# Kernel tuning notes

Hardware: AMD Instinct MI355X
Metric: run time of the kernel (lower is better)

The kernel has to match this reference:

```python
import jax, jax.numpy as jnp
import numpy as np

KS = 3
PAD = 1
N = KS * KS  # 9 sampling points per output location


def setup_inputs() -> dict:
    key = jax.random.key(0)
    k1, k2, k3 = jax.random.split(key, 3)
    b, c, H, W, outc = 4, 128, 64, 64, 128
    x = jax.random.normal(k1, (b, c, H, W), jnp.float32)
    offset = jax.random.normal(k2, (b, 2 * N, H, W), jnp.float32)
    weight = jax.random.normal(k3, (outc, c, KS, KS), jnp.float32) * 0.05
    return {"x": x, "offset": offset, "weight": weight}


def reference(x, offset, weight):
    b, c, H, W = x.shape
    h, w = offset.shape[2], offset.shape[3]
    # reorder interleaved (x,y,x,y,...) offset channels to (all x, all y)
    idx = jnp.concatenate([jnp.arange(0, 2 * N, 2), jnp.arange(1, 2 * N, 2)])
    offset = offset[:, idx]
    # zero padding
    xp = jnp.pad(x, ((0, 0), (0, 0), (PAD, PAD), (PAD, PAD)))
    Hp, Wp = H + 2 * PAD, W + 2 * PAD
    # kernel-relative offsets p_n: [1, 2N, 1, 1]
    r = np.arange(-(KS - 1) // 2, (KS - 1) // 2 + 1)
    pnx, pny = np.meshgrid(r, r, indexing='ij')
    p_n = jnp.asarray(np.concatenate([pnx.flatten(), pny.flatten()]).reshape(1, 2 * N, 1, 1), jnp.float32)
    # base grid p_0: [1, 2N, h, w], coords start at 1 (padded frame)
    p0x, p0y = np.meshgrid(np.arange(1, h + 1), np.arange(1, w + 1), indexing='ij')
    p_0 = jnp.asarray(np.concatenate([np.tile(p0x.reshape(1, 1, h, w), (1, N, 1, 1)),
                                      np.tile(p0y.reshape(1, 1, h, w), (1, N, 1, 1))], axis=1), jnp.float32)
    p = jnp.transpose(p_0 + p_n + offset, (0, 2, 3, 1))  # [b, h, w, 2N]
    px, py = p[..., :N], p[..., N:]
    fx, fy = jnp.floor(px), jnp.floor(py)
    # 4 corner integer coords, clamped to padded image
    q_lt_x = jnp.clip(fx, 0, Hp - 1).astype(jnp.int32)
    q_lt_y = jnp.clip(fy, 0, Wp - 1).astype(jnp.int32)
    q_rb_x = jnp.clip(fx + 1, 0, Hp - 1).astype(jnp.int32)
    q_rb_y = jnp.clip(fy + 1, 0, Wp - 1).astype(jnp.int32)
    # out-of-range mask: snap p to floor(p) there (matches original, incl. zero grad thru floor)
    mask_x = jax.lax.stop_gradient(((px < PAD) | (px > Hp - 1 - PAD)).astype(px.dtype))
    mask_y = jax.lax.stop_gradient(((py < PAD) | (py > Wp - 1 - PAD)).astype(py.dtype))
    px = px * (1 - mask_x) + fx * mask_x
    py = py * (1 - mask_y) + fy * mask_y
    px = jnp.clip(px, 0, Hp - 1)
    py = jnp.clip(py, 0, Wp - 1)
    qltx = q_lt_x.astype(px.dtype); qlty = q_lt_y.astype(px.dtype)
    qrbx = q_rb_x.astype(px.dtype); qrby = q_rb_y.astype(px.dtype)
    # bilinear weights: [b, h, w, N]
    g_lt = (1 + (qltx - px)) * (1 + (qlty - py))
    g_rb = (1 - (qrbx - px)) * (1 - (qrby - py))
    g_lb = (1 + (qltx - px)) * (1 - (qrby - py))
    g_rt = (1 - (qrbx - px)) * (1 + (qlty - py))

    xv = xp.reshape(b, c, Hp * Wp)

    def gather(qx, qy):
        lin = (qx * Wp + qy).reshape(b, 1, h * w * N)
        g = jnp.take_along_axis(xv, jnp.broadcast_to(lin, (b, c, h * w * N)), axis=2)
        return g.reshape(b, c, h, w, N)

    x_off = (g_lt[:, None] * gather(q_lt_x, q_lt_y)
             + g_rb[:, None] * gather(q_rb_x, q_rb_y)
             + g_lb[:, None] * gather(q_lt_x, q_rb_y)
             + g_rt[:, None] * gather(q_rb_x, q_lt_y))  # [b, c, h, w, N]
    # N = i*ks + j -> out[(h,i),(w,j)]
    xo = x_off.reshape(b, c, h, w, KS, KS).transpose(0, 1, 2, 4, 3, 5).reshape(b, c, h * KS, w * KS)
    out = jax.lax.conv_general_dilated(xo, weight, window_strides=(KS, KS), padding='VALID',
                                       dimension_numbers=('NCHW', 'OIHW', 'NCHW'))
    return out
```

## Files before the change

### kernel.cpp

```cpp
#include <hip/hip_runtime.h>


typedef __bf16  v8bf16 __attribute__((ext_vector_type(8)));
typedef __bf16  bf16x2 __attribute__((ext_vector_type(2)));
typedef __bf16  bf16x4 __attribute__((ext_vector_type(4)));
typedef float   f32x4  __attribute__((ext_vector_type(4)));
typedef unsigned short ushort4v __attribute__((ext_vector_type(4)));
typedef _Float16 half4v __attribute__((ext_vector_type(4)));

#define CIN  128
#define NPT  9
#define KTOT 1152
#define OC   128
#define PX   32
#define NDESC (NPT * PX)
#define KSTEPS 36
#define KSC  12
#define LDBc 392
#define DTOT (9 * 4 * 64 * 64)
#define PXR  64
#define LDR  392

#define PB_WFRAG 72
#define PB_XPOSE 1024
#define PB_DESC  576
#define PB_ZERO  2048
#define PB_TOTAL (PB_WFRAG + PB_XPOSE + PB_DESC + PB_ZERO)

__device__ __forceinline__ void desc_compute(const float* __restrict__ off, int t,
                                             uint4* __restrict__ desc) {
    int j   = t & 63;
    int i   = (t >> 6) & 63;
    int b   = (t >> 12) & 3;
    int tap = t >> 14;

    float ox = off[(((b * 18) + 2 * tap) << 12) + (i << 6) + j];
    float oy = off[(((b * 18) + 2 * tap + 1) << 12) + (i << 6) + j];
    float px = (float)(i + tap / 3) + ox;
    float py = (float)(j + tap % 3) + oy;
    float fx = floorf(px), fy = floorf(py);
    int qltx = (int)fminf(fmaxf(fx, 0.f), 65.f);
    int qlty = (int)fminf(fmaxf(fy, 0.f), 65.f);
    int qrbx = (int)fminf(fmaxf(fx + 1.f, 0.f), 65.f);
    int qrby = (int)fminf(fmaxf(fy + 1.f, 0.f), 65.f);
    if (px < 1.f || px > 64.f) px = fx;
    if (py < 1.f || py > 64.f) py = fy;
    px = fminf(fmaxf(px, 0.f), 65.f);
    py = fminf(fmaxf(py, 0.f), 65.f);
    float wxl = 1.f + (float)qltx - px;
    float wxr = 1.f - ((float)qrbx - px);
    float wyl = 1.f + (float)qlty - py;
    float wyr = 1.f - ((float)qrby - py);
    float g[4] = { wxl * wyl, wxr * wyr, wxl * wyr, wxr * wyl };
    int qx[4] = { qltx, qrbx, qltx, qrbx };
    int qy[4] = { qlty, qrby, qrby, qlty };
    unsigned short idx[4];
    half4v gh;
    #pragma unroll
    for (int cr = 0; cr < 4; ++cr) {
        bool inb = (qx[cr] >= 1) && (qx[cr] <= 64) && (qy[cr] >= 1) && (qy[cr] <= 64);
        idx[cr] = inb ? (unsigned short)((qx[cr] - 1) * 64 + (qy[cr] - 1)) : 0;
        gh[cr]  = inb ? (_Float16)g[cr] : (_Float16)0.f;
    }
    uint4 rec;
    rec.x = (unsigned)idx[0] | ((unsigned)idx[1] << 16);
    rec.y = (unsigned)idx[2] | ((unsigned)idx[3] << 16);
    __builtin_memcpy(&rec.z, &gh, 8);
    int d = (((b << 6) + i) * 64 + j) * 9 + tap;
    desc[d] = rec;
}

__global__ __launch_bounds__(256) void prep_kernel(
    const float* __restrict__ x, const float* __restrict__ off,
    const float* __restrict__ w, __bf16* __restrict__ wfrag,
    __bf16* __restrict__ xt, uint4* __restrict__ desc,
    float* __restrict__ out)
{
    __shared__ float tile[64][33];
    const int bid = blockIdx.x;
    const int tid = threadIdx.x;

    if (bid < PB_WFRAG) {
        int t = bid * 256 + tid;
        if (t < 8 * KSTEPS * 64) {
            int lane = t & 63;
            int ks   = (t >> 6) % KSTEPS;
            int ot   = t / (KSTEPS * 64);
            int o    = ot * 16 + (lane & 15);
            v8bf16 frag;
            #pragma unroll
            for (int e = 0; e < 8; ++e) {
                int k   = ks * 32 + (lane >> 4) * 8 + e;
                int tap = k >> 7, c = k & 127;
                frag[e] = (__bf16)w[(size_t)o * KTOT + c * NPT + tap];
            }
            *(v8bf16*)(wfrag + (size_t)t * 8) = frag;
        }
    } else if (bid < PB_WFRAG + PB_XPOSE) {
        const int bidx = bid - PB_WFRAG;
        const int b   = bidx >> 8;
        const int hw0 = ((bidx >> 2) & 63) * 64;
        const int c0  = (bidx & 3) * 32;
        #pragma unroll
        for (int r = 0; r < 8; ++r) {
            int c_l  = (tid >> 6) + r * 4;
            int hw_l = tid & 63;
            tile[hw_l][c_l] = x[((size_t)(b * CIN + c0 + c_l) << 12) + hw0 + hw_l];
        }
        __syncthreads();
        #pragma unroll
        for (int r = 0; r < 8; ++r) {
            int hw_l = (tid >> 5) + r * 8;
            int c_l  = tid & 31;
            xt[((size_t)(b * 4096 + hw0 + hw_l)) * CIN + c0 + c_l] = (__bf16)tile[hw_l][c_l];
        }
    } else if (bid < PB_WFRAG + PB_XPOSE + PB_DESC) {
        int t = (bid - PB_WFRAG - PB_XPOSE) * 256 + tid;
        if (t < DTOT) desc_compute(off, t, desc);
    } else {
        int t = (bid - PB_WFRAG - PB_XPOSE - PB_DESC) * 256 + tid;
        f32x4 z = {0.f, 0.f, 0.f, 0.f};
        *(f32x4*)(out + (size_t)t * 4) = z;
    }
}

__global__ __launch_bounds__(512, 6) void splitk_kernel(
    const uint4* __restrict__ desc, const __bf16* __restrict__ xt,
    const __bf16* __restrict__ wfrag, float* __restrict__ out)
{
    __shared__ __align__(16) __bf16 Bt[PXR][LDR];

    const int bidx = blockIdx.x;
    const int kh3 = bidx % 3;
    const int rest = bidx / 3;
    const int i   = rest & 63;
    const int b   = rest >> 6;
    const int tid = threadIdx.x;

    const int tap0 = kh3 * 3;

    const int l  = tid & 63;
    const int wv = tid >> 6;

    const __bf16* xtb = xt + (((size_t)b << 12) * CIN);
    const int pix_base = ((b << 6) + i) * 64;

    const int hh = l >> 5;
    const int ll = l & 31;
    #pragma unroll 3
    for (int m = 0; m < 12; ++m) {
        int dl = wv * 24 + 2 * m + hh;
        int tap_l = dl >> 6, p = dl & 63;
        int d = (pix_base + p) * 9 + tap0 + tap_l;
        uint4 q = desc[d];
        unsigned short idx[4] = { (unsigned short)(q.x & 0xffff), (unsigned short)(q.x >> 16),
                                  (unsigned short)(q.y & 0xffff), (unsigned short)(q.y >> 16) };
        half4v gh;
        __builtin_memcpy(&gh, &q.z, 8);
        float s0 = 0.f, s1 = 0.f, s2 = 0.f, s3 = 0.f;
        #pragma unroll
        for (int cr = 0; cr < 4; ++cr) {
            uint2 v = *(const uint2*)(xtb + (size_t)idx[cr] * CIN + 4 * ll);
            float c0v, c1v, c2v, c3v;
            unsigned int l0 = v.x << 16, h0 = v.x & 0xffff0000u;
            unsigned int l1 = v.y << 16, h1 = v.y & 0xffff0000u;
            __builtin_memcpy(&c0v, &l0, 4);
            __builtin_memcpy(&c1v, &h0, 4);
            __builtin_memcpy(&c2v, &l1, 4);
            __builtin_memcpy(&c3v, &h1, 4);
            float gf = (float)gh[cr];
            s0 += gf * c0v;
            s1 += gf * c1v;
            s2 += gf * c2v;
            s3 += gf * c3v;
        }
        bf16x4 pr = { (__bf16)s0, (__bf16)s1, (__bf16)s2, (__bf16)s3 };
        *(bf16x4*)&Bt[p][tap_l * CIN + 4 * ll] = pr;
    }
    __syncthreads();

    const int quad = l >> 4;
    const int lr   = l & 15;

    f32x4 acc0 = {0.f, 0.f, 0.f, 0.f};
    f32x4 acc1 = {0.f, 0.f, 0.f, 0.f};
    f32x4 acc2 = {0.f, 0.f, 0.f, 0.f};
    f32x4 acc3 = {0.f, 0.f, 0.f, 0.f};

    const __bf16* brow0 = &Bt[lr][quad * 8];
    const __bf16* brow1 = &Bt[16 + lr][quad * 8];
    const __bf16* brow2 = &Bt[32 + lr][quad * 8];
    const __bf16* brow3 = &Bt[48 + lr][quad * 8];

    #pragma unroll 3
    for (int ks = 0; ks < KSC; ++ks) {
        int ks_g = kh3 * KSC + ks;
        v8bf16 afrag = *(const v8bf16*)(wfrag + (((size_t)wv * KSTEPS + ks_g) * 64 + l) * 8);
        v8bf16 b0 = *(const v8bf16*)(brow0 + ks * 32);
        v8bf16 b1 = *(const v8bf16*)(brow1 + ks * 32);
        v8bf16 b2 = *(const v8bf16*)(brow2 + ks * 32);
        v8bf16 b3 = *(const v8bf16*)(brow3 + ks * 32);
        acc0 = __builtin_amdgcn_mfma_f32_16x16x32_bf16(afrag, b0, acc0, 0, 0, 0);
        acc1 = __builtin_amdgcn_mfma_f32_16x16x32_bf16(afrag, b1, acc1, 0, 0, 0);
        acc2 = __builtin_amdgcn_mfma_f32_16x16x32_bf16(afrag, b2, acc2, 0, 0, 0);
        acc3 = __builtin_amdgcn_mfma_f32_16x16x32_bf16(afrag, b3, acc3, 0, 0, 0);
    }

    int obase = wv * 16 + quad * 4;
    float* opb = out + (((size_t)(b * OC + obase)) << 12) + (i << 6) + lr;
    #pragma unroll
    for (int ph = 0; ph < 4; ++ph) {
        f32x4 a = (ph == 0) ? acc0 : (ph == 1) ? acc1 : (ph == 2) ? acc2 : acc3;
        float* op = opb + ph * 16;
        #pragma unroll
        for (int r = 0; r < 4; ++r)
            unsafeAtomicAdd(op + ((size_t)r << 12), a[r]);
    }
}

__global__ __launch_bounds__(512, 8) void deform_fused_kernel(
    const float* __restrict__ x, const float* __restrict__ off,
    const float* __restrict__ w, const __bf16* __restrict__ wfrag,
    const __bf16* __restrict__ xt, float* __restrict__ out, int mode)
{
    __shared__ __align__(16) __bf16 Bt[PX][LDBc];
    __shared__ __align__(8)  unsigned short sIdxP[NDESC][4];
    __shared__ __align__(8)  _Float16      sGP[NDESC][4];

    const int bidx = blockIdx.x;
    const int b   = bidx >> 8;
    const int i   = (bidx >> 2) & 63;
    const int j0  = ((bidx >> 1) & 1) * PX;
    const int oh  = bidx & 1;
    const int tid = threadIdx.x;

    if (tid < NDESC) {
        int k = tid >> 5, p = tid & 31;
        int j = j0 + p;
        float ox = off[(((b * 18) + 2 * k) * 64 + i) * 64 + j];
        float oy = off[(((b * 18) + 2 * k + 1) * 64 + i) * 64 + j];
        float px = (float)(i + k / 3) + ox;
        float py = (float)(j + k % 3) + oy;
        float fx = floorf(px), fy = floorf(py);
        int qltx = (int)fminf(fmaxf(fx, 0.f), 65.f);
        int qlty = (int)fminf(fmaxf(fy, 0.f), 65.f);
        int qrbx = (int)fminf(fmaxf(fx + 1.f, 0.f), 65.f);
        int qrby = (int)fminf(fmaxf(fy + 1.f, 0.f), 65.f);
        if (px < 1.f || px > 64.f) px = fx;
        if (py < 1.f || py > 64.f) py = fy;
        px = fminf(fmaxf(px, 0.f), 65.f);
        py = fminf(fmaxf(py, 0.f), 65.f);
        float wxl = 1.f + (float)qltx - px;
        float wxr = 1.f - ((float)qrbx - px);
        float wyl = 1.f + (float)qlty - py;
        float wyr = 1.f - ((float)qrby - py);
        float g[4] = { wxl * wyl, wxr * wyr, wxl * wyr, wxr * wyl };
        int qx[4] = { qltx, qrbx, qltx, qrbx };
        int qy[4] = { qlty, qrby, qrby, qlty };
        #pragma unroll
        for (int cr = 0; cr < 4; ++cr) {
            bool inb = (qx[cr] >= 1) && (qx[cr] <= 64) && (qy[cr] >= 1) && (qy[cr] <= 64);
            sIdxP[tid][cr] = inb ? (unsigned short)((qx[cr] - 1) * 64 + (qy[cr] - 1)) : 0;
            sGP[tid][cr]   = inb ? (_Float16)g[cr] : (_Float16)0.f;
        }
    }
    __syncthreads();

    const int l    = tid & 63;
    const int wv   = tid >> 6;
    const int ot   = oh * 4 + (wv & 3);
    const int ph   = wv >> 2;
    const int quad = l >> 4;
    const int lr   = l & 15;

    f32x4 acc = {0.f, 0.f, 0.f, 0.f};
    const __bf16* xtb = xt + ((size_t)b * 4096) * CIN;
    const float*  xb  = x + ((size_t)b * CIN << 12);
    const __bf16* brow = &Bt[ph * 16 + lr][quad * 8];

    for (int t = 0; t < 3; ++t) {
        if (mode == 2) {
            #pragma unroll 4
            for (int dd = 0; dd < KSC; ++dd) {
                int dl = wv * KSC + dd;
                int tap_l = dl >> 5, p = dl & 31;
                int d = t * 96 + dl;
                ushort4v id = *(const ushort4v*)&sIdxP[d][0];
                half4v   gh = *(const half4v*)&sGP[d][0];
                float s0 = 0.f, s1 = 0.f;
                #pragma unroll
                for (int cr = 0; cr < 4; ++cr) {
                    unsigned int v = *(const unsigned int*)(xtb + (size_t)id[cr] * CIN + 2 * l);
                    float c0v, c1v;
                    unsigned int lo = v << 16, hi = v & 0xffff0000u;
                    __builtin_memcpy(&c0v, &lo, 4);
                    __builtin_memcpy(&c1v, &hi, 4);
                    float gf = (float)gh[cr];
                    s0 += gf * c0v;
                    s1 += gf * c1v;
                }
                bf16x2 pr = { (__bf16)s0, (__bf16)s1 };
                *(bf16x2*)&Bt[p][tap_l * CIN + 2 * l] = pr;
            }
        } else {
            for (int dd = 0; dd < KSC; ++dd) {
                int dl = wv * KSC + dd;
                int tap_l = dl >> 5, p = dl & 31;
                int d = t * 96 + dl;
                ushort4v id = *(const ushort4v*)&sIdxP[d][0];
                half4v   gh = *(const half4v*)&sGP[d][0];
                float s0 = 0.f, s1 = 0.f;
                #pragma unroll
                for (int cr = 0; cr < 4; ++cr) {
                    float gf = (float)gh[cr];
                    s0 += gf * xb[((size_t)(2 * l) << 12) + id[cr]];
                    s1 += gf * xb[((size_t)(2 * l + 1) << 12) + id[cr]];
                }
                bf16x2 pr = { (__bf16)s0, (__bf16)s1 };
                *(bf16x2*)&Bt[p][tap_l * CIN + 2 * l] = pr;
            }
        }
        __syncthreads();

        #pragma unroll 4
        for (int ks = 0; ks < KSC; ++ks) {
            int ks_g = t * KSC + ks;
            v8bf16 bfrag = *(const v8bf16*)(brow + ks * 32);
            v8bf16 afrag;
            if (mode >= 1) {
                afrag = *(const v8bf16*)(wfrag + (((size_t)ot * KSTEPS + ks_g) * 64 + l) * 8);
            } else {
                int o = ot * 16 + lr;
                #pragma unroll
                for (int e = 0; e < 8; ++e) {
                    int k = ks_g * 32 + quad * 8 + e;
                    int tap = k >> 7, c = k & 127;
                    afrag[e] = (__bf16)w[(size_t)o * KTOT + c * NPT + tap];
                }
            }
            acc = __builtin_amdgcn_mfma_f32_16x16x32_bf16(afrag, bfrag, acc, 0, 0, 0);
        }
        if (t < 2) __syncthreads();
    }

    {
        int obase = ot * 16 + quad * 4;
        float* op = out + (((size_t)(b * OC + obase)) << 12) + (i << 6) + j0 + ph * 16 + lr;
        #pragma unroll
        for (int r = 0; r < 4; ++r)
            op[(size_t)r << 12] = acc[r];
    }
}

__global__ __launch_bounds__(256) void wfrag_kernel(const float* __restrict__ w,
                                                    __bf16* __restrict__ wfrag) {
    int t = blockIdx.x * 256 + threadIdx.x;
    if (t >= 8 * KSTEPS * 64) return;
    int lane = t & 63;
    int ks   = (t >> 6) % KSTEPS;
    int ot   = t / (KSTEPS * 64);
    int o    = ot * 16 + (lane & 15);
    v8bf16 frag;
    #pragma unroll
    for (int e = 0; e < 8; ++e) {
        int k   = ks * 32 + (lane >> 4) * 8 + e;
        int tap = k >> 7, c = k & 127;
        frag[e] = (__bf16)w[(size_t)o * KTOT + c * NPT + tap];
    }
    *(v8bf16*)(wfrag + (size_t)t * 8) = frag;
}

__global__ __launch_bounds__(256) void xpose_kernel(const float* __restrict__ x,
                                                    __bf16* __restrict__ xt) {
    __shared__ float tile[64][33];
    const int bidx = blockIdx.x;
    const int b   = bidx >> 8;
    const int hw0 = ((bidx >> 2) & 63) * 64;
    const int c0  = (bidx & 3) * 32;
    const int tid = threadIdx.x;
    #pragma unroll
    for (int r = 0; r < 8; ++r) {
        int c_l  = (tid >> 6) + r * 4;
        int hw_l = tid & 63;
        tile[hw_l][c_l] = x[((size_t)(b * CIN + c0 + c_l) << 12) + hw0 + hw_l];
    }
    __syncthreads();
    #pragma unroll
    for (int r = 0; r < 8; ++r) {
        int hw_l = (tid >> 5) + r * 8;
        int c_l  = tid & 31;
        xt[((size_t)(b * 4096 + hw0 + hw_l)) * CIN + c0 + c_l] = (__bf16)tile[hw_l][c_l];
    }
}

extern "C" void kernel_launch(void* const* d_in, const int* in_sizes, int n_in,
                              void* d_out, int out_size, void* d_ws, size_t ws_size,
                              hipStream_t stream) {
    const float* x   = (const float*)d_in[0];
    const float* off = (const float*)d_in[1];
    const float* w   = (const float*)d_in[2];
    float* out = (float*)d_out;

    const size_t wfrag_bytes = (size_t)OC * KTOT * sizeof(__bf16);
    const size_t xt_bytes    = (size_t)4 * 4096 * CIN * sizeof(__bf16);
    const size_t desc_bytes  = (size_t)DTOT * 16;

    int mode = 0;
    if (ws_size >= wfrag_bytes + xt_bytes + desc_bytes) mode = 3;
    else if (ws_size >= wfrag_bytes + xt_bytes) mode = 2;
    else if (ws_size >= wfrag_bytes) mode = 1;

    __bf16* wfrag = (__bf16*)d_ws;
    __bf16* xt    = (__bf16*)((char*)d_ws + wfrag_bytes);
    uint4*  desc  = (uint4*) ((char*)d_ws + wfrag_bytes + xt_bytes);

    if (mode == 3) {
        prep_kernel<<<PB_TOTAL, 256, 0, stream>>>(x, off, w, wfrag, xt, desc, out);
        splitk_kernel<<<4 * 64 * 3, 512, 0, stream>>>(desc, xt, wfrag, out);
    } else {
        if (mode >= 1)
            wfrag_kernel<<<(8 * KSTEPS * 64 + 255) / 256, 256, 0, stream>>>(w, wfrag);
        if (mode >= 2)
            xpose_kernel<<<4 * 64 * 4, 256, 0, stream>>>(x, xt);
        deform_fused_kernel<<<4 * 64 * 2 * 2, 512, 0, stream>>>(x, off, w, wfrag, xt, out, mode);
    }
}
```

Baseline: 101.7 us.

## Widen gather loads to 16B, prefetch descriptors, and remap block order by batch

The gather phase now has each lane load 8 bf16 channels (16-byte loads) instead of 4, so 16 lanes cover one descriptor and the loop runs 6 iterations instead of 12. All 6 descriptors are loaded up front to raise memory-level parallelism. Block indices are remapped so adjacent blocks interleave batches differently, which is meant to change L2 locality across the grid. The costs are more registers (six uint4 descriptors plus eight accumulators per lane) and possible occupancy loss under launch_bounds(512,6).

```diff
diff --git a/kernel.cpp b/kernel.cpp
--- a/kernel.cpp
+++ b/kernel.cpp
@@ -3,7 +3,6 @@
 
 typedef __bf16  v8bf16 __attribute__((ext_vector_type(8)));
 typedef __bf16  bf16x2 __attribute__((ext_vector_type(2)));
-typedef __bf16  bf16x4 __attribute__((ext_vector_type(4)));
 typedef float   f32x4  __attribute__((ext_vector_type(4)));
 typedef unsigned short ushort4v __attribute__((ext_vector_type(4)));
 typedef _Float16 half4v __attribute__((ext_vector_type(4)));
@@ -131,11 +130,11 @@
     __shared__ __align__(16) __bf16 Bt[PXR][LDR];
 
     const int bidx = blockIdx.x;
-    const int kh3 = bidx % 3;
-    const int rest = bidx / 3;
-    const int i   = rest & 63;
-    const int b   = rest >> 6;
-    const int tid = threadIdx.x;
+    const int b    = (bidx & 7) >> 1;
+    const int sub  = ((bidx >> 3) << 1) | (bidx & 1);
+    const int kh3  = sub % 3;
+    const int i    = sub / 3;
+    const int tid  = threadIdx.x;
 
     const int tap0 = kh3 * 3;
 
@@ -145,37 +144,51 @@
     const __bf16* xtb = xt + (((size_t)b << 12) * CIN);
     const int pix_base = ((b << 6) + i) * 64;
 
-    const int hh = l >> 5;
-    const int ll = l & 31;
-    #pragma unroll 3
-    for (int m = 0; m < 12; ++m) {
-        int dl = wv * 24 + 2 * m + hh;
-        int tap_l = dl >> 6, p = dl & 63;
-        int d = (pix_base + p) * 9 + tap0 + tap_l;
-        uint4 q = desc[d];
-        unsigned short idx[4] = { (unsigned short)(q.x & 0xffff), (unsigned short)(q.x >> 16),
-                                  (unsigned short)(q.y & 0xffff), (unsigned short)(q.y >> 16) };
-        half4v gh;
-        __builtin_memcpy(&gh, &q.z, 8);
-        float s0 = 0.f, s1 = 0.f, s2 = 0.f, s3 = 0.f;
-        #pragma unroll
-        for (int cr = 0; cr < 4; ++cr) {
-            uint2 v = *(const uint2*)(xtb + (size_t)idx[cr] * CIN + 4 * ll);
-            float c0v, c1v, c2v, c3v;
-            unsigned int l0 = v.x << 16, h0 = v.x & 0xffff0000u;
-            unsigned int l1 = v.y << 16, h1 = v.y & 0xffff0000u;
-            __builtin_memcpy(&c0v, &l0, 4);
-            __builtin_memcpy(&c1v, &h0, 4);
-            __builtin_memcpy(&c2v, &l1, 4);
-            __builtin_memcpy(&c3v, &h1, 4);
-            float gf = (float)gh[cr];
-            s0 += gf * c0v;
-            s1 += gf * c1v;
-            s2 += gf * c2v;
-            s3 += gf * c3v;
-        }
-        bf16x4 pr = { (__bf16)s0, (__bf16)s1, (__bf16)s2, (__bf16)s3 };
-        *(bf16x4*)&Bt[p][tap_l * CIN + 4 * ll] = pr;
+    {
+        const int q  = l >> 4;
+        const int ll = l & 15;
+
+        uint4 qd[6];
+        int   pp[6], tt[6];
+        #pragma unroll
+        for (int m = 0; m < 6; ++m) {
+            int dl = wv * 24 + m * 4 + q;
+            tt[m] = dl >> 6;
+            pp[m] = dl & 63;
+            int d = (pix_base + pp[m]) * 9 + tap0 + tt[m];
+            qd[m] = desc[d];
+        }
+
+        #pragma unroll
+        for (int m = 0; m < 6; ++m) {
+            unsigned short idx[4] = {
+                (unsigned short)(qd[m].x & 0xffff), (unsigned short)(qd[m].x >> 16),
+                (unsigned short)(qd[m].y & 0xffff), (unsigned short)(qd[m].y >> 16) };
+            half4v gh;
+            unsigned int zz[2] = { qd[m].z, qd[m].w };
+            __builtin_memcpy(&gh, &zz, 8);
+
+            float s[8] = {0.f,0.f,0.f,0.f,0.f,0.f,0.f,0.f};
+            #pragma unroll
+            for (int cr = 0; cr < 4; ++cr) {
+                uint4 v = *(const uint4*)(xtb + (size_t)idx[cr] * CIN + 8 * ll);
+                float gf = (float)gh[cr];
+                unsigned int dw[4] = { v.x, v.y, v.z, v.w };
+                #pragma unroll
+                for (int e = 0; e < 4; ++e) {
+                    float clo, chi;
+                    unsigned int lo = dw[e] << 16, hi = dw[e] & 0xffff0000u;
+                    __builtin_memcpy(&clo, &lo, 4);
+                    __builtin_memcpy(&chi, &hi, 4);
+                    s[2 * e]     += gf * clo;
+                    s[2 * e + 1] += gf * chi;
+                }
+            }
+            v8bf16 pr;
+            #pragma unroll
+            for (int e = 0; e < 8; ++e) pr[e] = (__bf16)s[e];
+            *(v8bf16*)&Bt[pp[m]][tt[m] * CIN + 8 * ll] = pr;
+        }
     }
     __syncthreads();
 
```

After: 95.55 us. 1.06x faster.
